# Kernel tuning notes

Measured on AMD Instinct MI355X. Metric: run time of the kernel, lower is better.

## Reference

```python
import jax, jax.numpy as jnp
import numpy as np

ALPHA = 0.1        # axis_aligned_projection threshold
NEG_INF = -1e30    # large negative used for masking (softmax-equivalent to -inf)


def axis_aligned_projection(x, alpha=ALPHA):
    x_abs = jnp.abs(x)
    max_vals = jnp.max(x_abs, axis=-1, keepdims=True)
    axis_weights = jnp.where(x_abs >= alpha * max_vals, x_abs, 0.0)
    return axis_weights * jnp.sign(x)


def setup_inputs() -> dict:
    key = jax.random.key(0)
    kq, kk, kv = jax.random.split(key, 3)
    B, L, H, E = 4, 2048, 8, 64
    S, D = L, E
    queries = jax.random.normal(kq, (B, L, H, E), dtype=jnp.float32)
    keys = jax.random.normal(kk, (B, S, H, E), dtype=jnp.float32)
    values = jax.random.normal(kv, (B, S, H, D), dtype=jnp.float32)
    # TriangularCausalMask: True strictly above the diagonal -> masked out
    causal = jnp.triu(jnp.ones((L, S), dtype=jnp.bool_), k=1)
    attn_mask = jnp.broadcast_to(causal[None, None], (B, 1, L, S))
    return {"queries": queries, "keys": keys, "values": values, "attn_mask": attn_mask}


def reference(queries, keys, values, attn_mask):
    B, L, H, E = queries.shape
    scale = 1.0 / jnp.sqrt(jnp.float32(E))
    q = axis_aligned_projection(queries)
    k = axis_aligned_projection(keys)
    # [B,H,L,S] dense scores (the module materializes the full matrix)
    scores = jnp.einsum('blhe,bshe->bhls', q, k)
    scores = jnp.where(attn_mask, NEG_INF, scores)
    A = jax.nn.softmax(scale * scores, axis=-1)  # dropout is identity in eval mode
    V = jnp.einsum('bhls,bshd->blhd', A, values)
    return V
```

## Files before the change

### kernel.cpp

```cpp
#include <hip/hip_runtime.h>
#include <hip/hip_bf16.h>
#include <stdint.h>

#define B_ 4
#define L_ 2048
#define H_ 8
#define E_ 64
#define ALPHA 0.1f
#define LOG2E 1.44269504088896f
#define QSCALE (0.125f * LOG2E)


typedef float f32x4 __attribute__((ext_vector_type(4)));
typedef short bf16x8 __attribute__((ext_vector_type(8)));
typedef short bf16x4 __attribute__((ext_vector_type(4)));
typedef uint32_t u32;
typedef unsigned short u16;
typedef u32 u32x2 __attribute__((ext_vector_type(2)));

__device__ __forceinline__ u16 f2bf(float f) {
    u32 x = __builtin_bit_cast(u32, f);
    u32 r = x + 0x7fffu + ((x >> 16) & 1u);
    return (u16)(r >> 16);
}

__device__ __forceinline__ u32 pk2bf(float a, float b) {
    u32 ua = __builtin_bit_cast(u32, a) + 0x8000u;
    u32 ub = __builtin_bit_cast(u32, b) + 0x8000u;
    return (ua >> 16) | (ub & 0xffff0000u);
}

__device__ __forceinline__ f32x4 mfma16x16x16bf16(bf16x4 a, bf16x4 b, f32x4 c) {
#if __has_builtin(__builtin_amdgcn_mfma_f32_16x16x16bf16_1k)
    return __builtin_amdgcn_mfma_f32_16x16x16bf16_1k(a, b, c, 0, 0, 0);
#elif __has_builtin(__builtin_amdgcn_mfma_f32_16x16x16_bf16)
    return __builtin_amdgcn_mfma_f32_16x16x16_bf16(a, b, c, 0, 0, 0);
#else
    f32x4 d;
    asm volatile("v_mfma_f32_16x16x16_bf16 %0, %1, %2, %3"
                 : "=v"(d) : "v"(a), "v"(b), "v"(c));
    return d;
#endif
}

__device__ __forceinline__ void dma16(const u16* g, u16* l) {
    __builtin_amdgcn_global_load_lds(
        (const __attribute__((address_space(1))) void*)g,
        (__attribute__((address_space(3))) void*)l, 16, 0, 0);
}

__global__ __launch_bounds__(256) void prep_kernel(const float* __restrict__ qin,
                                                   const float* __restrict__ kin,
                                                   const float* __restrict__ vin,
                                                   u16* __restrict__ qp,
                                                   u16* __restrict__ kp,
                                                   u16* __restrict__ vt) {
    __shared__ u16 tile[64][66];
    if (blockIdx.x < 4096) {
        const int RG = (B_ * L_ * H_) / 8;
        int wave = threadIdx.x >> 6, lane = threadIdx.x & 63;
        int g = blockIdx.x * 4 + wave;
        const float* src;
        u16* dst;
        int gr;
        float sc;
        bool isq;
        if (g < RG) { src = qin; dst = qp; gr = g; sc = QSCALE; isq = true; }
        else        { src = kin; dst = kp; gr = g - RG; sc = 1.0f; isq = false; }

        int rig = lane >> 3;
        int j = lane & 7;
        int c = j * 4;
        int row = gr * 8 + rig;

        const float* rp = src + (size_t)row * 64;
        float4 v0 = *(const float4*)(rp + c);
        float4 v1 = *(const float4*)(rp + c + 32);
        float f[8] = {v0.x, v0.y, v0.z, v0.w, v1.x, v1.y, v1.z, v1.w};

        float mx = 0.f;
#pragma unroll
        for (int i = 0; i < 8; ++i) mx = fmaxf(mx, fabsf(f[i]));
#pragma unroll
        for (int m = 1; m < 8; m <<= 1) mx = fmaxf(mx, __shfl_xor(mx, m));
        float thr = ALPHA * mx;

        u16 o[8];
#pragma unroll
        for (int i = 0; i < 8; ++i)
            o[i] = (fabsf(f[i]) >= thr) ? f2bf(f[i] * sc) : (u16)0;

        int b = row >> 14;
        int l = (row >> 3) & (L_ - 1);
        int h = row & 7;
        int e0, e1;
        if (isq) {
            e0 = c;
            e1 = c + 32;
        } else {
            int l7 = l & 7;
            e0 = (((j >> 1) ^ l7) << 3) + ((j & 1) << 2);
            e1 = ((((j >> 1) + 4) ^ l7) << 3) + ((j & 1) << 2);
        }
        u16* orow = dst + ((size_t)(b * H_ + h) * L_ + l) * 64;
        uint2 p0 = {(u32)o[0] | ((u32)o[1] << 16), (u32)o[2] | ((u32)o[3] << 16)};
        uint2 p1 = {(u32)o[4] | ((u32)o[5] << 16), (u32)o[6] | ((u32)o[7] << 16)};
        *(uint2*)(orow + e0) = p0;
        *(uint2*)(orow + e1) = p1;
    } else {
        int bx = blockIdx.x - 4096;
        int bh = bx >> 5, sblk = bx & 31;
        int b = bh >> 3, h = bh & 7;
        int t = threadIdx.x;
        int s0 = sblk * 64;

#pragma unroll
        for (int p = 0; p < 2; ++p) {
            int sl = p * 32 + (t >> 3);
            int c = (t & 7) * 4;
            const float* rp = vin + (((size_t)(b * L_ + s0 + sl)) * H_ + h) * 64;
            float4 a = *(const float4*)(rp + c);
            float4 bb = *(const float4*)(rp + c + 32);
            u32* d0 = (u32*)&tile[sl][c];
            d0[0] = (u32)f2bf(a.x) | ((u32)f2bf(a.y) << 16);
            d0[1] = (u32)f2bf(a.z) | ((u32)f2bf(a.w) << 16);
            u32* d1 = (u32*)&tile[sl][c + 32];
            d1[0] = (u32)f2bf(bb.x) | ((u32)f2bf(bb.y) << 16);
            d1[1] = (u32)f2bf(bb.z) | ((u32)f2bf(bb.w) << 16);
        }
        __syncthreads();
#pragma unroll
        for (int p = 0; p < 2; ++p) {
            int d = p * 32 + (t >> 3);
            int c16 = t & 7;
            int sc2 = c16 * 8;
            u16 o[8];
#pragma unroll
            for (int i = 0; i < 8; ++i) o[i] = tile[sc2 + i][d];
            u32 w0 = (u32)o[0] | ((u32)o[1] << 16);
            u32 w1 = (u32)o[2] | ((u32)o[3] << 16);
            u32 w2 = (u32)o[4] | ((u32)o[5] << 16);
            u32 w3 = (u32)o[6] | ((u32)o[7] << 16);
            uint4 val;
            if (d & 1) { val.x = w2; val.y = w3; val.z = w0; val.w = w1; }
            else       { val.x = w0; val.y = w1; val.z = w2; val.w = w3; }
            int pc = c16 ^ ((d >> 1) & 7);
            *(uint4*)(vt + ((size_t)(bh * 32 + sblk) * 64 + d) * 64 + pc * 8) = val;
        }
    }
}

__global__ __launch_bounds__(256, 4) void flash_kernel(const u16* __restrict__ Qp,
                                                       const u16* __restrict__ Kp,
                                                       const u16* __restrict__ Vt,
                                                       float* __restrict__ out) {
    __shared__ u16 kbuf[2][64 * 64];
    __shared__ u16 vbuf[2][64 * 64];
    int t = threadIdx.x;
    int wave = t >> 6, lane = t & 63;
    int bh = blockIdx.x & 31;
    int r5 = blockIdx.x >> 5;
    int g = r5 & 7, kr = r5 >> 3;
    int qq = (kr == 0) ? (31 - g) : (kr == 1) ? (16 + g) : (kr == 2) ? (15 - g) : g;
    int lo = lane & 15, quad = lane >> 4;
    int lo7 = lo & 7;
    int q0 = qq * 64 + wave * 16;
    int b = bh >> 3, h = bh & 7;

    int kc0 = (quad ^ lo7) << 3;
    int kc1 = ((quad + 4) ^ lo7) << 3;

    const u16* kTiles = Kp + (size_t)bh * L_ * 64;
    const u16* vTiles = Vt + (size_t)bh * 32 * 64 * 64;

    auto stage = [&](int sb, int buf) {
        const u16* kg = kTiles + (size_t)sb * 64;
        const u16* vg = vTiles + (size_t)(sb >> 6) * 64 * 64;
        u16* kl = kbuf[buf];
        u16* vl = vbuf[buf];
        for (int i = wave; i < 16; i += 4) {
            if (i < 8) dma16(kg + i * 512 + lane * 8, kl + i * 512);
            else       dma16(vg + (i - 8) * 512 + lane * 8, vl + (i - 8) * 512);
        }
    };

    const u16* qbase = Qp + ((size_t)bh * L_ + q0 + lo) * 64 + quad * 8;
    bf16x8 aQ0 = *(const bf16x8*)(qbase);
    bf16x8 aQ1 = *(const bf16x8*)(qbase + 32);

    f32x4 o[4];
#pragma unroll
    for (int ni = 0; ni < 4; ++ni) o[ni] = (f32x4){0.f, 0.f, 0.f, 0.f};
    float ls = 0.f;

    auto frag_proc = [&](const u16* ks, const u16* vs, int sub, bool diag) {
        const u16* krow = ks + ((sub * 16 + lo) << 6);
        bf16x8 k0 = *(const bf16x8*)(krow + kc0);
        bf16x8 k1 = *(const bf16x8*)(krow + kc1);
        f32x4 S = {0.f, 0.f, 0.f, 0.f};
        S = __builtin_amdgcn_mfma_f32_16x16x32_bf16(k0, aQ0, S, 0, 0, 0);
        S = __builtin_amdgcn_mfma_f32_16x16x32_bf16(k1, aQ1, S, 0, 0, 0);

        int vsw = ((sub * 4 + quad) ^ lo) << 2;
        bf16x4 vf[4];
#pragma unroll
        for (int ni = 0; ni < 4; ++ni)
            vf[ni] = *(const bf16x4*)(vs + ((ni * 16 + lo) << 6) + vsw);

        float P[4];
#pragma unroll
        for (int r = 0; r < 4; ++r) {
            float e = __builtin_amdgcn_exp2f(S[r]);
            P[r] = (diag && (quad * 4 + r > lo)) ? 0.f : e;
        }
        ls += (P[0] + P[1]) + (P[2] + P[3]);
        u32x2 pk = {pk2bf(P[0], P[1]), pk2bf(P[2], P[3])};
        bf16x4 aP = __builtin_bit_cast(bf16x4, pk);
#pragma unroll
        for (int ni = 0; ni < 4; ++ni)
            o[ni] = mfma16x16x16bf16(aP, vf[ni], o[ni]);
    };

    stage(0, 0);
    __syncthreads();

    for (int kt = 0; kt < qq; ++kt) {
        int cur = kt & 1;
        stage((kt + 1) << 6, cur ^ 1);
        const u16* ks = kbuf[cur];
        const u16* vs = vbuf[cur];
#pragma unroll
        for (int sub = 0; sub < 4; ++sub) frag_proc(ks, vs, sub, false);
        __syncthreads();
    }

    {
        int cur = qq & 1;
        const u16* ks = kbuf[cur];
        const u16* vs = vbuf[cur];
        for (int sub = 0; sub < wave; ++sub) frag_proc(ks, vs, sub, false);
        frag_proc(ks, vs, wave, true);
    }

    ls += __shfl_xor(ls, 16);
    ls += __shfl_xor(ls, 32);
#pragma unroll
    for (int r = 0; r < 4; ++r) {
        float lr = __shfl(ls, quad * 4 + r);
        float inv = 1.0f / lr;
        int q = q0 + quad * 4 + r;
        float* ob = out + (((size_t)(b * L_ + q)) * H_ + h) * 64 + lo;
        ob[0]  = o[0][r] * inv;
        ob[16] = o[1][r] * inv;
        ob[32] = o[2][r] * inv;
        ob[48] = o[3][r] * inv;
    }
}

extern "C" void kernel_launch(void* const* d_in, const int* in_sizes, int n_in,
                              void* d_out, int out_size, void* d_ws, size_t ws_size,
                              hipStream_t stream) {
    const float* q = (const float*)d_in[0];
    const float* k = (const float*)d_in[1];
    const float* v = (const float*)d_in[2];
    float* out = (float*)d_out;

    const size_t QSZ = (size_t)B_ * H_ * L_ * 64;
    u16* qp = (u16*)d_ws;
    u16* kp = qp + QSZ;
    u16* vt = kp + QSZ;

    prep_kernel<<<5120, 256, 0, stream>>>(q, k, v, qp, kp, vt);
    flash_kernel<<<1024, 256, 0, stream>>>(qp, kp, vt, out);
}
```

Baseline: 163.8 us.

## Triple-buffer K tiles and prefetch two ahead with partial vmcnt waits

Splits tile staging into separate K and V loads, adds a third LDS buffer for K, and prefetches K two tiles ahead while V stays one tile ahead. The __syncthreads is replaced by inline s_waitcnt vmcnt(2) plus s_barrier, so the newest K prefetch can stay in flight across the barrier. This aims to hide more global-to-LDS latency. It raises LDS use by 8 KB per block, which may reduce occupancy, and it depends on the order in which the DMAs are issued for the partial waitcnt to be correct.

```diff
diff --git a/kernel.cpp b/kernel.cpp
--- a/kernel.cpp
+++ b/kernel.cpp
@@ -154,7 +154,7 @@
                                                        const u16* __restrict__ Kp,
                                                        const u16* __restrict__ Vt,
                                                        float* __restrict__ out) {
-    __shared__ u16 kbuf[2][64 * 64];
+    __shared__ u16 kbuf[3][64 * 64];
     __shared__ u16 vbuf[2][64 * 64];
     int t = threadIdx.x;
     int wave = t >> 6, lane = t & 63;
@@ -173,20 +173,23 @@
     const u16* kTiles = Kp + (size_t)bh * L_ * 64;
     const u16* vTiles = Vt + (size_t)bh * 32 * 64 * 64;
 
-    auto stage = [&](int sb, int buf) {
-        const u16* kg = kTiles + (size_t)sb * 64;
-        const u16* vg = vTiles + (size_t)(sb >> 6) * 64 * 64;
+    auto stageK = [&](int kt, int buf) {
+        const u16* kg = kTiles + (size_t)kt * 4096;
         u16* kl = kbuf[buf];
+        dma16(kg + wave * 512 + lane * 8, kl + wave * 512);
+        dma16(kg + (wave + 4) * 512 + lane * 8, kl + (wave + 4) * 512);
+    };
+    auto stageV = [&](int kt, int buf) {
+        const u16* vg = vTiles + (size_t)kt * 4096;
         u16* vl = vbuf[buf];
-        for (int i = wave; i < 16; i += 4) {
-            if (i < 8) dma16(kg + i * 512 + lane * 8, kl + i * 512);
-            else       dma16(vg + (i - 8) * 512 + lane * 8, vl + (i - 8) * 512);
-        }
+        dma16(vg + wave * 512 + lane * 8, vl + wave * 512);
+        dma16(vg + (wave + 4) * 512 + lane * 8, vl + (wave + 4) * 512);
     };
 
     const u16* qbase = Qp + ((size_t)bh * L_ + q0 + lo) * 64 + quad * 8;
     bf16x8 aQ0 = *(const bf16x8*)(qbase);
     bf16x8 aQ1 = *(const bf16x8*)(qbase + 32);
+    asm volatile("" :: "v"(aQ0), "v"(aQ1));
 
     f32x4 o[4];
 #pragma unroll
@@ -221,23 +224,37 @@
             o[ni] = mfma16x16x16bf16(aP, vf[ni], o[ni]);
     };
 
-    stage(0, 0);
-    __syncthreads();
+    stageV(0, 0);
+    asm volatile("" ::: "memory");
+    stageK(0, 0);
+    if (qq >= 1) {
+        stageK(1, 1);
+        asm volatile("s_waitcnt vmcnt(2)\n\ts_barrier" ::: "memory");
+    } else {
+        asm volatile("s_waitcnt vmcnt(0)\n\ts_barrier" ::: "memory");
+    }
+
+    int kb0 = 0, kb1 = 1, kb2 = 2;
 
     for (int kt = 0; kt < qq; ++kt) {
-        int cur = kt & 1;
-        stage((kt + 1) << 6, cur ^ 1);
-        const u16* ks = kbuf[cur];
-        const u16* vs = vbuf[cur];
+        stageV(kt + 1, (kt + 1) & 1);
+        asm volatile("" ::: "memory");
+        bool haveK2 = (kt + 2 <= qq);
+        if (haveK2) stageK(kt + 2, kb2);
+
+        const u16* ks = kbuf[kb0];
+        const u16* vs = vbuf[kt & 1];
 #pragma unroll
         for (int sub = 0; sub < 4; ++sub) frag_proc(ks, vs, sub, false);
-        __syncthreads();
+
+        if (haveK2) asm volatile("s_waitcnt vmcnt(2)\n\ts_barrier" ::: "memory");
+        else        asm volatile("s_waitcnt vmcnt(0)\n\ts_barrier" ::: "memory");
+        int tmp = kb0; kb0 = kb1; kb1 = kb2; kb2 = tmp;
     }
 
     {
-        int cur = qq & 1;
-        const u16* ks = kbuf[cur];
-        const u16* vs = vbuf[cur];
+        const u16* ks = kbuf[kb0];
+        const u16* vs = vbuf[qq & 1];
         for (int sub = 0; sub < wave; ++sub) frag_proc(ks, vs, sub, false);
         frag_proc(ks, vs, wave, true);
     }
```

Measured after the change: 168.0 us. 2.5% more time.

## Split key subtiles across waves, each wave covering all query groups

Applied to the files above, without the earlier changes.

Each wave now owns one 16-key slice of every 64-key tile and computes scores for all four 16-row query groups, instead of owning 16 queries and looping over all four key slices. Each wave therefore loads only its own K/V fragments and keeps four Q fragments plus sixteen output accumulators in registers. The per-wave partial outputs and row sums are combined through shared memory (reusing the K/V buffers) and written as vectorized rows. This raises register pressure (launch bounds drop from 4 to 3 blocks per CU) and adds a cross-wave reduction epilogue with extra barriers.

```diff
diff --git a/kernel.cpp b/kernel.cpp
--- a/kernel.cpp
+++ b/kernel.cpp
@@ -150,32 +150,34 @@
     }
 }
 
-__global__ __launch_bounds__(256, 4) void flash_kernel(const u16* __restrict__ Qp,
+__global__ __launch_bounds__(256, 3) void flash_kernel(const u16* __restrict__ Qp,
                                                        const u16* __restrict__ Kp,
                                                        const u16* __restrict__ Vt,
                                                        float* __restrict__ out) {
     __shared__ u16 kbuf[2][64 * 64];
     __shared__ u16 vbuf[2][64 * 64];
+    __shared__ float lsh[2][64];
     int t = threadIdx.x;
     int wave = t >> 6, lane = t & 63;
     int bh = blockIdx.x & 31;
     int r5 = blockIdx.x >> 5;
-    int g = r5 & 7, kr = r5 >> 3;
-    int qq = (kr == 0) ? (31 - g) : (kr == 1) ? (16 + g) : (kr == 2) ? (15 - g) : g;
+    int g8 = r5 & 7, kr = r5 >> 3;
+    int qq = (kr == 0) ? (31 - g8) : (kr == 1) ? (16 + g8) : (kr == 2) ? (15 - g8) : g8;
     int lo = lane & 15, quad = lane >> 4;
     int lo7 = lo & 7;
-    int q0 = qq * 64 + wave * 16;
     int b = bh >> 3, h = bh & 7;
 
     int kc0 = (quad ^ lo7) << 3;
     int kc1 = ((quad + 4) ^ lo7) << 3;
+    int krowoff = ((wave * 16 + lo) << 6);
+    int vsw = ((wave * 4 + quad) ^ lo) << 2;
 
     const u16* kTiles = Kp + (size_t)bh * L_ * 64;
     const u16* vTiles = Vt + (size_t)bh * 32 * 64 * 64;
 
-    auto stage = [&](int sb, int buf) {
-        const u16* kg = kTiles + (size_t)sb * 64;
-        const u16* vg = vTiles + (size_t)(sb >> 6) * 64 * 64;
+    auto stage = [&](int kt, int buf) {
+        const u16* kg = kTiles + (size_t)kt * 4096;
+        const u16* vg = vTiles + (size_t)kt * 4096;
         u16* kl = kbuf[buf];
         u16* vl = vbuf[buf];
         for (int i = wave; i < 16; i += 4) {
@@ -184,41 +186,54 @@
         }
     };
 
-    const u16* qbase = Qp + ((size_t)bh * L_ + q0 + lo) * 64 + quad * 8;
-    bf16x8 aQ0 = *(const bf16x8*)(qbase);
-    bf16x8 aQ1 = *(const bf16x8*)(qbase + 32);
-
-    f32x4 o[4];
-#pragma unroll
-    for (int ni = 0; ni < 4; ++ni) o[ni] = (f32x4){0.f, 0.f, 0.f, 0.f};
-    float ls = 0.f;
-
-    auto frag_proc = [&](const u16* ks, const u16* vs, int sub, bool diag) {
-        const u16* krow = ks + ((sub * 16 + lo) << 6);
+    bf16x8 aQ0[4], aQ1[4];
+#pragma unroll
+    for (int g = 0; g < 4; ++g) {
+        const u16* qb = Qp + ((size_t)bh * L_ + qq * 64 + g * 16 + lo) * 64 + quad * 8;
+        aQ0[g] = *(const bf16x8*)(qb);
+        aQ1[g] = *(const bf16x8*)(qb + 32);
+    }
+    asm volatile("" :: "v"(aQ0[0]), "v"(aQ1[0]), "v"(aQ0[1]), "v"(aQ1[1]),
+                       "v"(aQ0[2]), "v"(aQ1[2]), "v"(aQ0[3]), "v"(aQ1[3]));
+
+    f32x4 o[4][4];
+#pragma unroll
+    for (int g = 0; g < 4; ++g)
+#pragma unroll
+        for (int ni = 0; ni < 4; ++ni) o[g][ni] = (f32x4){0.f, 0.f, 0.f, 0.f};
+    float lsg[4] = {0.f, 0.f, 0.f, 0.f};
+
+    auto tile_proc = [&](const u16* ks, const u16* vs) {
+        const u16* krow = ks + krowoff;
         bf16x8 k0 = *(const bf16x8*)(krow + kc0);
         bf16x8 k1 = *(const bf16x8*)(krow + kc1);
-        f32x4 S = {0.f, 0.f, 0.f, 0.f};
-        S = __builtin_amdgcn_mfma_f32_16x16x32_bf16(k0, aQ0, S, 0, 0, 0);
-        S = __builtin_amdgcn_mfma_f32_16x16x32_bf16(k1, aQ1, S, 0, 0, 0);
-
-        int vsw = ((sub * 4 + quad) ^ lo) << 2;
         bf16x4 vf[4];
 #pragma unroll
         for (int ni = 0; ni < 4; ++ni)
             vf[ni] = *(const bf16x4*)(vs + ((ni * 16 + lo) << 6) + vsw);
-
-        float P[4];
-#pragma unroll
-        for (int r = 0; r < 4; ++r) {
-            float e = __builtin_amdgcn_exp2f(S[r]);
-            P[r] = (diag && (quad * 4 + r > lo)) ? 0.f : e;
-        }
-        ls += (P[0] + P[1]) + (P[2] + P[3]);
-        u32x2 pk = {pk2bf(P[0], P[1]), pk2bf(P[2], P[3])};
-        bf16x4 aP = __builtin_bit_cast(bf16x4, pk);
-#pragma unroll
-        for (int ni = 0; ni < 4; ++ni)
-            o[ni] = mfma16x16x16bf16(aP, vf[ni], o[ni]);
+        f32x4 S[4];
+#pragma unroll
+        for (int g = 0; g < 4; ++g) {
+            f32x4 acc = {0.f, 0.f, 0.f, 0.f};
+            acc = __builtin_amdgcn_mfma_f32_16x16x32_bf16(k0, aQ0[g], acc, 0, 0, 0);
+            S[g] = __builtin_amdgcn_mfma_f32_16x16x32_bf16(k1, aQ1[g], acc, 0, 0, 0);
+        }
+        bf16x4 aP[4];
+#pragma unroll
+        for (int g = 0; g < 4; ++g) {
+            float P0 = __builtin_amdgcn_exp2f(S[g][0]);
+            float P1 = __builtin_amdgcn_exp2f(S[g][1]);
+            float P2 = __builtin_amdgcn_exp2f(S[g][2]);
+            float P3 = __builtin_amdgcn_exp2f(S[g][3]);
+            lsg[g] += (P0 + P1) + (P2 + P3);
+            u32x2 pk = {pk2bf(P0, P1), pk2bf(P2, P3)};
+            aP[g] = __builtin_bit_cast(bf16x4, pk);
+        }
+#pragma unroll
+        for (int g = 0; g < 4; ++g)
+#pragma unroll
+            for (int ni = 0; ni < 4; ++ni)
+                o[g][ni] = mfma16x16x16bf16(aP[g], vf[ni], o[g][ni]);
     };
 
     stage(0, 0);
@@ -226,11 +241,8 @@
 
     for (int kt = 0; kt < qq; ++kt) {
         int cur = kt & 1;
-        stage((kt + 1) << 6, cur ^ 1);
-        const u16* ks = kbuf[cur];
-        const u16* vs = vbuf[cur];
-#pragma unroll
-        for (int sub = 0; sub < 4; ++sub) frag_proc(ks, vs, sub, false);
+        stage(kt + 1, cur ^ 1);
+        tile_proc(kbuf[cur], vbuf[cur]);
         __syncthreads();
     }
 
@@ -238,22 +250,84 @@
         int cur = qq & 1;
         const u16* ks = kbuf[cur];
         const u16* vs = vbuf[cur];
-        for (int sub = 0; sub < wave; ++sub) frag_proc(ks, vs, sub, false);
-        frag_proc(ks, vs, wave, true);
-    }
-
-    ls += __shfl_xor(ls, 16);
-    ls += __shfl_xor(ls, 32);
-#pragma unroll
-    for (int r = 0; r < 4; ++r) {
-        float lr = __shfl(ls, quad * 4 + r);
-        float inv = 1.0f / lr;
-        int q = q0 + quad * 4 + r;
-        float* ob = out + (((size_t)(b * L_ + q)) * H_ + h) * 64 + lo;
-        ob[0]  = o[0][r] * inv;
-        ob[16] = o[1][r] * inv;
-        ob[32] = o[2][r] * inv;
-        ob[48] = o[3][r] * inv;
+        const u16* krow = ks + krowoff;
+        bf16x8 k0 = *(const bf16x8*)(krow + kc0);
+        bf16x8 k1 = *(const bf16x8*)(krow + kc1);
+        bf16x4 vf[4];
+#pragma unroll
+        for (int ni = 0; ni < 4; ++ni)
+            vf[ni] = *(const bf16x4*)(vs + ((ni * 16 + lo) << 6) + vsw);
+#pragma unroll
+        for (int g = 0; g < 4; ++g) {
+            if (g < wave) continue;
+            f32x4 acc = {0.f, 0.f, 0.f, 0.f};
+            acc = __builtin_amdgcn_mfma_f32_16x16x32_bf16(k0, aQ0[g], acc, 0, 0, 0);
+            f32x4 S = __builtin_amdgcn_mfma_f32_16x16x32_bf16(k1, aQ1[g], acc, 0, 0, 0);
+            float P[4];
+#pragma unroll
+            for (int r = 0; r < 4; ++r) {
+                float e = __builtin_amdgcn_exp2f(S[r]);
+                P[r] = (g == wave && (quad * 4 + r > lo)) ? 0.f : e;
+            }
+            lsg[g] += (P[0] + P[1]) + (P[2] + P[3]);
+            u32x2 pk = {pk2bf(P[0], P[1]), pk2bf(P[2], P[3])};
+            bf16x4 aP = __builtin_bit_cast(bf16x4, pk);
+#pragma unroll
+            for (int ni = 0; ni < 4; ++ni)
+                o[g][ni] = mfma16x16x16bf16(aP, vf[ni], o[g][ni]);
+        }
+    }
+
+#pragma unroll
+    for (int g = 0; g < 4; ++g) {
+        lsg[g] += __shfl_xor(lsg[g], 16);
+        lsg[g] += __shfl_xor(lsg[g], 32);
+    }
+    __syncthreads();
+    float* OA = (float*)&kbuf[0][0];
+    float* OB = (float*)&vbuf[0][0];
+    if (wave < 2) {
+        float* R = wave ? OB : OA;
+#pragma unroll
+        for (int g = 0; g < 4; ++g)
+#pragma unroll
+            for (int ni = 0; ni < 4; ++ni)
+#pragma unroll
+                for (int r = 0; r < 4; ++r)
+                    R[(g * 16 + quad * 4 + r) * 64 + ni * 16 + lo] = o[g][ni][r];
+        if (quad == 0)
+#pragma unroll
+            for (int g = 0; g < 4; ++g) lsh[wave][g * 16 + lo] = lsg[g];
+    }
+    __syncthreads();
+    if (wave >= 2) {
+        float* R = (wave == 3) ? OB : OA;
+#pragma unroll
+        for (int g = 0; g < 4; ++g)
+#pragma unroll
+            for (int ni = 0; ni < 4; ++ni)
+#pragma unroll
+                for (int r = 0; r < 4; ++r)
+                    R[(g * 16 + quad * 4 + r) * 64 + ni * 16 + lo] += o[g][ni][r];
+        if (quad == 0)
+#pragma unroll
+            for (int g = 0; g < 4; ++g) lsh[wave - 2][g * 16 + lo] += lsg[g];
+    }
+    __syncthreads();
+    {
+        int qrow = wave * 16 + (lane >> 2);
+        int d0 = (lane & 3) * 16;
+        float inv = 1.0f / (lsh[0][qrow] + lsh[1][qrow]);
+        float* ob = out + (((size_t)(b * L_ + qq * 64 + qrow)) * H_ + h) * 64 + d0;
+        const float* pa = OA + qrow * 64 + d0;
+        const float* pb = OB + qrow * 64 + d0;
+#pragma unroll
+        for (int j = 0; j < 4; ++j) {
+            f32x4 va = *(const f32x4*)(pa + j * 4);
+            f32x4 vb = *(const f32x4*)(pb + j * 4);
+            f32x4 vr = (va + vb) * inv;
+            *(f32x4*)(ob + j * 4) = vr;
+        }
     }
 }
 
```

Measured after the change: 168.5 us. +2.9%, slower.
